# Performance work log

Measured on AMD Instinct MI355X. Metric: run time of the kernel, lower is better.

## Reference

```python
import jax, jax.numpy as jnp
import numpy as np

NUM_LAYERS = 3
DROPOUT = 0.1
N_NODES = 100000
N_EDGES = 3200000
D_FEAT = 128


def setup_inputs() -> dict:
    key = jax.random.key(0)
    k1, k2, k3, k4 = jax.random.split(key, 4)
    question_embs = jax.random.normal(k1, (N_NODES, D_FEAT), dtype=jnp.float32)
    edge_rows = jax.random.randint(k2, (N_EDGES,), 0, N_NODES, dtype=jnp.int32)
    edge_cols = jax.random.randint(k3, (N_EDGES,), 0, N_NODES, dtype=jnp.int32)
    edge_vals = jax.random.uniform(k4, (N_EDGES,), dtype=jnp.float32)
    return {"question_embs": question_embs, "edge_rows": edge_rows,
            "edge_cols": edge_cols, "edge_vals": edge_vals}


def _spmm(edge_rows, edge_cols, edge_vals, x):
    # sparse [N,N] @ dense [N,D] in COO form: out[r] += v * x[c]
    msgs = edge_vals[:, None] * x[edge_cols]        # [E, D]
    return jax.ops.segment_sum(msgs, edge_rows, num_segments=N_NODES)


def reference(question_embs, edge_rows, edge_cols, edge_vals):
    keep = 1.0 - DROPOUT
    base_key = jax.random.key(42)
    acc = question_embs                  # running sum over layer outputs
    prev = question_embs
    for layer in range(NUM_LAYERS):
        h = _spmm(edge_rows, edge_cols, edge_vals, prev)
        h = h + prev                     # residual to previous layer output
        mask = jax.random.bernoulli(jax.random.fold_in(base_key, layer),
                                    keep, h.shape)
        h = jnp.where(mask, h / keep, 0.0)  # F.dropout semantics (training)
        acc = acc + h
        prev = h
    return acc / (NUM_LAYERS + 1)        # mean over stacked layer outputs
```

## Files before the change

kernel.cpp:

```cpp
#include <hip/hip_runtime.h>
#include <stdint.h>

#define NN 100000
#define DF 128
#define NE 3200000
#define NELEM (NN * DF)
#define NBUCK 391
#define BCAP 12288
#define BSTRIDE 16
#define EPB 4096
#define NBINBLK ((NE + EPB - 1) / EPB)
#define OVF_CAP 65536

__host__ __device__ __forceinline__ void tf2x32(uint32_t& x0, uint32_t& x1,
                                                uint32_t k0, uint32_t k1) {
  uint32_t ks2 = k0 ^ k1 ^ 0x1BD11BDAu;
  x0 += k0; x1 += k1;
#define TF_RND(r) { x0 += x1; x1 = (x1 << (r)) | (x1 >> (32 - (r))); x1 ^= x0; }
  TF_RND(13) TF_RND(15) TF_RND(26) TF_RND(6)
  x0 += k1;  x1 += ks2 + 1u;
  TF_RND(17) TF_RND(29) TF_RND(16) TF_RND(24)
  x0 += ks2; x1 += k0 + 2u;
  TF_RND(13) TF_RND(15) TF_RND(26) TF_RND(6)
  x0 += k0;  x1 += k1 + 3u;
  TF_RND(17) TF_RND(29) TF_RND(16) TF_RND(24)
  x0 += k1;  x1 += ks2 + 4u;
  TF_RND(13) TF_RND(15) TF_RND(26) TF_RND(6)
  x0 += ks2; x1 += k0 + 5u;
#undef TF_RND
}

__device__ __forceinline__ bool keep_elem(uint32_t kA, uint32_t kB, uint32_t idx) {
  uint32_t x0 = 0u, x1 = idx;
  tf2x32(x0, x1, kA, kB);
  uint32_t bits = x0 ^ x1;
  float u = __uint_as_float((bits >> 9) | 0x3f800000u) - 1.0f;
  return u < 0.9f;
}

__device__ __forceinline__ uint16_t f2bf(float f) {
  uint32_t x = __float_as_uint(f);
  uint32_t r = x + 0x7fffu + ((x >> 16) & 1u);
  return (uint16_t)(r >> 16);
}

__device__ __forceinline__ uint64_t pack_edge(int row, int col, float val) {
  return ((uint64_t)(uint32_t)row << 47) | ((uint64_t)(uint32_t)col << 30) |
         (uint64_t)(__float_as_uint(val) >> 2);
}

__device__ __forceinline__ uint32_t pack_csr(int col, float v) {
  int m = (int)(v * 32768.0f + 0.5f);
  if (m > 32767) m = 32767;
  return ((uint32_t)col << 15) | (uint32_t)m;
}

__global__ __launch_bounds__(256) void binfill2_kernel(
    const int* __restrict__ rows, const int* __restrict__ cols,
    const float* __restrict__ vals,
    int* __restrict__ bcnt,
    int* __restrict__ ovf_cnt, int* __restrict__ row_cnt_ovf,
    uint64_t* __restrict__ staging, uint64_t* __restrict__ ovf) {
  __shared__ int lcnt[NBUCK];
  __shared__ int lcur[NBUCK];
  int t = threadIdx.x;
  for (int i = t; i < NBUCK; i += 256) lcnt[i] = 0;
  __syncthreads();

  int base = blockIdx.x * EPB;
  int rr[16];
#pragma unroll
  for (int k = 0; k < 16; ++k) {
    int e = base + k * 256 + t;
    rr[k] = (e < NE) ? rows[e] : -1;
    if (rr[k] >= 0) atomicAdd(&lcnt[rr[k] >> 8], 1);
  }
  __syncthreads();
  for (int i = t; i < NBUCK; i += 256)
    lcur[i] = atomicAdd(&bcnt[i * BSTRIDE], lcnt[i]);
  __syncthreads();
#pragma unroll
  for (int k = 0; k < 16; ++k) {
    if (rr[k] < 0) continue;
    int e = base + k * 256 + t;
    int row = rr[k];
    int b = row >> 8;
    uint64_t packed = pack_edge(row, cols[e], vals[e]);
    int slot = atomicAdd(&lcur[b], 1);
    if (slot < BCAP) {
      staging[(size_t)b * BCAP + slot] = packed;
    } else {
      int o = atomicAdd(ovf_cnt, 1);
      if (o < OVF_CAP) ovf[o] = packed;
      atomicAdd(&row_cnt_ovf[row], 1);
    }
  }
}

__global__ __launch_bounds__(512) void scan_bsums_kernel(const int* __restrict__ bcnt,
                                                         int* __restrict__ boff) {
  __shared__ int lds[512];
  int tid = threadIdx.x;
  int v = (tid < NBUCK) ? bcnt[tid * BSTRIDE] : 0;
  lds[tid] = v;
  __syncthreads();
#pragma unroll
  for (int off = 1; off < 512; off <<= 1) {
    int add = (tid >= off) ? lds[tid - off] : 0;
    __syncthreads();
    lds[tid] += add;
    __syncthreads();
  }
  if (tid < NBUCK) boff[tid] = lds[tid] - v;
}

__global__ __launch_bounds__(256) void scatter_csr2_kernel(
    const int* __restrict__ bcnt, const int* __restrict__ boff,
    const int* __restrict__ row_cnt_ovf,
    const uint64_t* __restrict__ staging,
    int* __restrict__ row_ptr, int* __restrict__ row_fill,
    uint32_t* __restrict__ csr) {
  __shared__ int scnt[256];
  __shared__ int lds[256];
  __shared__ int lcur[256];
  int b = blockIdx.x;
  int t = threadIdx.x;
  int g = b * 256 + t;
  int n_tot = bcnt[b * BSTRIDE];
  int n_stg = min(n_tot, BCAP);
  const uint64_t* src = staging + (size_t)b * BCAP;

  scnt[t] = 0;
  __syncthreads();
  for (int i = t; i < n_stg; i += 256)
    atomicAdd(&scnt[(int)(src[i] >> 47) & 255], 1);
  __syncthreads();
  int ovfc = (g < NN) ? row_cnt_ovf[g] : 0;
  int v = scnt[t] + ovfc;
  lds[t] = v;
  __syncthreads();
#pragma unroll
  for (int off = 1; off < 256; off <<= 1) {
    int add = (t >= off) ? lds[t - off] : 0;
    __syncthreads();
    lds[t] += add;
    __syncthreads();
  }
  int excl = lds[t] - v;
  int bo = boff[b];
  if (g <= NN) row_ptr[g] = bo + excl;
  if (g < NN) row_fill[g] = bo + excl + scnt[t];
  lcur[t] = excl;
  __syncthreads();
  for (int i = t; i < n_stg; i += 256) {
    uint64_t p = src[i];
    int rl = (int)(p >> 47) & 255;
    int col = (int)((p >> 30) & 0x1FFFFu);
    float vv = __uint_as_float(((uint32_t)p & 0x3FFFFFFFu) << 2);
    int pos = bo + atomicAdd(&lcur[rl], 1);
    csr[pos] = pack_csr(col, vv);
  }
}

__global__ __launch_bounds__(256) void ovf_drain_kernel(
    const int* __restrict__ ovf_cnt, const uint64_t* __restrict__ ovf,
    int* __restrict__ row_fill, uint32_t* __restrict__ csr) {
  int n = min(*ovf_cnt, OVF_CAP);
  for (int i = threadIdx.x; i < n; i += 256) {
    uint64_t p = ovf[i];
    int row = (int)(p >> 47);
    int col = (int)((p >> 30) & 0x1FFFFu);
    float vv = __uint_as_float(((uint32_t)p & 0x3FFFFFFFu) << 2);
    int pos = atomicAdd(&row_fill[row], 1);
    csr[pos] = pack_csr(col, vv);
  }
}

__global__ __launch_bounds__(256) void convert_kernel(const float4* __restrict__ src,
                                                      ushort4* __restrict__ dst) {
  int i = blockIdx.x * 256 + threadIdx.x;
  if (i < NELEM / 4) {
    float4 v = src[i];
    dst[i] = make_ushort4(f2bf(v.x), f2bf(v.y), f2bf(v.z), f2bf(v.w));
  }
}

template <int MODE>
__global__ __launch_bounds__(256) void spmm_layer_kernel(
    const int* __restrict__ row_ptr,
    const uint32_t* __restrict__ csr,
    const uint32_t* __restrict__ xb,
    const uint32_t* __restrict__ qb,
    const uint32_t* __restrict__ h1b,
    uint32_t* __restrict__ hb_out,
    float2* __restrict__ outv,
    uint32_t kA, uint32_t kB) {
  int r = __builtin_amdgcn_readfirstlane(blockIdx.x * 4 + (threadIdx.x >> 6));
  if (r >= NN) return;
  int lane = threadIdx.x & 63;
  int beg = row_ptr[r], end = row_ptr[r + 1];

  float s0a = 0.f, s1a = 0.f, s0b = 0.f, s1b = 0.f;
  int j = beg;
  int n8 = beg + ((end - beg) & ~7);
  for (; j < n8; j += 8) {
    uint32_t cv[8];
#pragma unroll
    for (int u = 0; u < 8; ++u) cv[u] = csr[j + u];
    uint32_t t[8];
#pragma unroll
    for (int u = 0; u < 8; ++u) {
      const uint32_t* p = xb + (size_t)(cv[u] >> 15) * 64;
      t[u] = p[lane];
    }
#pragma unroll
    for (int u = 0; u < 8; ++u) {
      float v = (float)(cv[u] & 0x7FFFu) * (1.0f / 32768.0f);
      float lo = __uint_as_float(t[u] << 16);
      float hi = __uint_as_float(t[u] & 0xFFFF0000u);
      if (u & 1) { s0b += v * lo; s1b += v * hi; }
      else       { s0a += v * lo; s1a += v * hi; }
    }
  }
  for (; j < end; ++j) {
    uint32_t cv = csr[j];
    float v = (float)(cv & 0x7FFFu) * (1.0f / 32768.0f);
    const uint32_t* p = xb + (size_t)(cv >> 15) * 64;
    uint32_t t = p[lane];
    s0a += v * __uint_as_float(t << 16);
    s1a += v * __uint_as_float(t & 0xFFFF0000u);
  }
  float s0 = s0a + s0b, s1 = s1a + s1b;

  int oi = r * 64 + lane;
  uint32_t pw = xb[oi];
  float p0 = __uint_as_float(pw << 16);
  float p1 = __uint_as_float(pw & 0xFFFF0000u);

  uint32_t base = (uint32_t)r * 128u + (uint32_t)lane * 2u;
  float t0 = s0 + p0, t1 = s1 + p1;
  float h0 = keep_elem(kA, kB, base)      ? t0 * (1.0f / 0.9f) : 0.0f;
  float h1 = keep_elem(kA, kB, base + 1u) ? t1 * (1.0f / 0.9f) : 0.0f;

  if (MODE < 2) {
    hb_out[oi] = (uint32_t)f2bf(h0) | ((uint32_t)f2bf(h1) << 16);
  } else {
    uint32_t qw = qb[oi];
    uint32_t hw = h1b[oi];
    float q0 = __uint_as_float(qw << 16), q1 = __uint_as_float(qw & 0xFFFF0000u);
    float a0 = __uint_as_float(hw << 16), a1 = __uint_as_float(hw & 0xFFFF0000u);
    outv[oi] = make_float2((q0 + a0 + p0 + h0) * 0.25f,
                           (q1 + a1 + p1 + h1) * 0.25f);
  }
}

extern "C" void kernel_launch(void* const* d_in, const int* in_sizes, int n_in,
                              void* d_out, int out_size, void* d_ws, size_t ws_size,
                              hipStream_t stream) {
  const float* q   = (const float*)d_in[0];
  const int* rows  = (const int*)d_in[1];
  const int* cols  = (const int*)d_in[2];
  const float* vls = (const float*)d_in[3];
  float* out = (float*)d_out;

  uint32_t kA[3], kB[3];
  for (int l = 0; l < 3; ++l) {
    uint32_t x0 = 0u, x1 = (uint32_t)l;
    tf2x32(x0, x1, 0u, 42u);
    kA[l] = x0; kB[l] = x1;
  }

  uint16_t* xb_q = (uint16_t*)d_ws;
  uint16_t* hb1  = xb_q + NELEM;
  uint16_t* hb2  = hb1 + NELEM;
  uint64_t* staging = (uint64_t*)hb1;
  uint32_t* csr  = (uint32_t*)(hb2 + NELEM);
  int* row_ptr   = (int*)(csr + NE);
  int* boff      = row_ptr + NN + 1;
  int* row_fill  = boff + NBUCK;
  int* row_cnt_ovf = row_fill + NN;
  int* bcnt      = row_cnt_ovf + NN;
  int* ovf_cnt   = bcnt + NBUCK * BSTRIDE;
  uint64_t* ovf  = (uint64_t*)(((uintptr_t)(ovf_cnt + 1) + 7) & ~(uintptr_t)7);

  dim3 blk(256);

  hipMemsetAsync(row_cnt_ovf, 0, (size_t)(NN + NBUCK * BSTRIDE + 1) * 4, stream);
  convert_kernel<<<NELEM / 4 / 256, blk, 0, stream>>>((const float4*)q, (ushort4*)xb_q);
  binfill2_kernel<<<NBINBLK, blk, 0, stream>>>(
      rows, cols, vls, bcnt, ovf_cnt, row_cnt_ovf, staging, ovf);
  scan_bsums_kernel<<<1, 512, 0, stream>>>(bcnt, boff);
  scatter_csr2_kernel<<<NBUCK, blk, 0, stream>>>(
      bcnt, boff, row_cnt_ovf, staging, row_ptr, row_fill, csr);
  ovf_drain_kernel<<<1, blk, 0, stream>>>(ovf_cnt, ovf, row_fill, csr);

  const int grid = NN / 4;
  spmm_layer_kernel<0><<<grid, blk, 0, stream>>>(
      row_ptr, csr, (const uint32_t*)xb_q, nullptr, nullptr,
      (uint32_t*)hb1, nullptr, kA[0], kB[0]);
  spmm_layer_kernel<1><<<grid, blk, 0, stream>>>(
      row_ptr, csr, (const uint32_t*)hb1, nullptr, nullptr,
      (uint32_t*)hb2, nullptr, kA[1], kB[1]);
  spmm_layer_kernel<2><<<grid, blk, 0, stream>>>(
      row_ptr, csr, (const uint32_t*)hb2, (const uint32_t*)xb_q,
      (const uint32_t*)hb1, nullptr, (float2*)out, kA[2], kB[2]);
}
```

Before: 445.3 us.

## Split SpMM into feature-half passes with two rows per wavefront

Each SpMM layer now runs as two launches, each covering one 64-feature half of the bf16 rows. A wavefront handles two rows at once, 32 lanes per row. The intent is to shrink the gathered working set per pass (half of each row, 128 bytes) so it stays in cache better, and to fold the value scaling out of the inner loop. The cost is reading the CSR indices twice per layer, divergent row lengths within a wavefront (the loop runs to the longer row), and twice as many launches.

```diff
diff --git a/kernel.cpp b/kernel.cpp
--- a/kernel.cpp
+++ b/kernel.cpp
@@ -185,8 +185,8 @@
   }
 }
 
-template <int MODE>
-__global__ __launch_bounds__(256) void spmm_layer_kernel(
+template <int MODE, int PASS>
+__global__ __launch_bounds__(256) void spmm_half_kernel(
     const int* __restrict__ row_ptr,
     const uint32_t* __restrict__ csr,
     const uint32_t* __restrict__ xb,
@@ -195,49 +195,65 @@
     uint32_t* __restrict__ hb_out,
     float2* __restrict__ outv,
     uint32_t kA, uint32_t kB) {
-  int r = __builtin_amdgcn_readfirstlane(blockIdx.x * 4 + (threadIdx.x >> 6));
-  if (r >= NN) return;
+  int pr = __builtin_amdgcn_readfirstlane(blockIdx.x * 4 + (threadIdx.x >> 6));
+  int rA = pr * 2;
   int lane = threadIdx.x & 63;
-  int beg = row_ptr[r], end = row_ptr[r + 1];
-
-  float s0a = 0.f, s1a = 0.f, s0b = 0.f, s1b = 0.f;
-  int j = beg;
-  int n8 = beg + ((end - beg) & ~7);
-  for (; j < n8; j += 8) {
-    uint32_t cv[8];
-#pragma unroll
-    for (int u = 0; u < 8; ++u) cv[u] = csr[j + u];
-    uint32_t t[8];
+  int l = lane & 31;
+  int half = lane >> 5;
+
+  int begA = row_ptr[rA];
+  int endA = row_ptr[rA + 1];
+  int endB = row_ptr[rA + 2];
+  int lenA = endA - begA, lenB = endB - endA;
+  const uint32_t* csrA = csr + begA;
+  const uint32_t* csrB = csr + endA;
+  int ml = lenA > lenB ? lenA : lenB;
+
+  const char* xbase = (const char*)xb;
+  uint32_t loff = (uint32_t)(PASS * 128 + (l << 2));
+
+  float s0 = 0.f, s1 = 0.f;
+  int j = 0, ml8 = ml & ~7;
+  for (; j < ml8; j += 8) {
+    uint32_t cw[8];
 #pragma unroll
     for (int u = 0; u < 8; ++u) {
-      const uint32_t* p = xb + (size_t)(cv[u] >> 15) * 64;
-      t[u] = p[lane];
+      uint32_t a = csrA[j + u]; a = (j + u < lenA) ? a : 0u;
+      uint32_t b = csrB[j + u]; b = (j + u < lenB) ? b : 0u;
+      cw[u] = half ? b : a;
     }
+    uint32_t ta[8];
 #pragma unroll
     for (int u = 0; u < 8; ++u) {
-      float v = (float)(cv[u] & 0x7FFFu) * (1.0f / 32768.0f);
-      float lo = __uint_as_float(t[u] << 16);
-      float hi = __uint_as_float(t[u] & 0xFFFF0000u);
-      if (u & 1) { s0b += v * lo; s1b += v * hi; }
-      else       { s0a += v * lo; s1a += v * hi; }
+      uint32_t off = ((cw[u] >> 15) << 8) + loff;
+      ta[u] = *(const uint32_t*)(xbase + off);
     }
-  }
-  for (; j < end; ++j) {
-    uint32_t cv = csr[j];
-    float v = (float)(cv & 0x7FFFu) * (1.0f / 32768.0f);
-    const uint32_t* p = xb + (size_t)(cv >> 15) * 64;
-    uint32_t t = p[lane];
-    s0a += v * __uint_as_float(t << 16);
-    s1a += v * __uint_as_float(t & 0xFFFF0000u);
-  }
-  float s0 = s0a + s0b, s1 = s1a + s1b;
-
-  int oi = r * 64 + lane;
+#pragma unroll
+    for (int u = 0; u < 8; ++u) {
+      float v = (float)(cw[u] & 0x7FFFu);
+      s0 += v * __uint_as_float(ta[u] << 16);
+      s1 += v * __uint_as_float(ta[u] & 0xFFFF0000u);
+    }
+  }
+  for (; j < ml; ++j) {
+    uint32_t a = csrA[j]; a = (j < lenA) ? a : 0u;
+    uint32_t b = csrB[j]; b = (j < lenB) ? b : 0u;
+    uint32_t cw = half ? b : a;
+    uint32_t t = *(const uint32_t*)(xbase + (((cw >> 15) << 8) + loff));
+    float v = (float)(cw & 0x7FFFu);
+    s0 += v * __uint_as_float(t << 16);
+    s1 += v * __uint_as_float(t & 0xFFFF0000u);
+  }
+  s0 *= (1.0f / 32768.0f);
+  s1 *= (1.0f / 32768.0f);
+
+  int r = rA + half;
+  int oi = r * 64 + PASS * 32 + l;
   uint32_t pw = xb[oi];
   float p0 = __uint_as_float(pw << 16);
   float p1 = __uint_as_float(pw & 0xFFFF0000u);
 
-  uint32_t base = (uint32_t)r * 128u + (uint32_t)lane * 2u;
+  uint32_t base = (uint32_t)r * 128u + (uint32_t)(PASS * 64) + (uint32_t)(l << 1);
   float t0 = s0 + p0, t1 = s1 + p1;
   float h0 = keep_elem(kA, kB, base)      ? t0 * (1.0f / 0.9f) : 0.0f;
   float h1 = keep_elem(kA, kB, base + 1u) ? t1 * (1.0f / 0.9f) : 0.0f;
@@ -294,14 +310,21 @@
       bcnt, boff, row_cnt_ovf, staging, row_ptr, row_fill, csr);
   ovf_drain_kernel<<<1, blk, 0, stream>>>(ovf_cnt, ovf, row_fill, csr);
 
-  const int grid = NN / 4;
-  spmm_layer_kernel<0><<<grid, blk, 0, stream>>>(
-      row_ptr, csr, (const uint32_t*)xb_q, nullptr, nullptr,
-      (uint32_t*)hb1, nullptr, kA[0], kB[0]);
-  spmm_layer_kernel<1><<<grid, blk, 0, stream>>>(
-      row_ptr, csr, (const uint32_t*)hb1, nullptr, nullptr,
-      (uint32_t*)hb2, nullptr, kA[1], kB[1]);
-  spmm_layer_kernel<2><<<grid, blk, 0, stream>>>(
-      row_ptr, csr, (const uint32_t*)hb2, (const uint32_t*)xb_q,
-      (const uint32_t*)hb1, nullptr, (float2*)out, kA[2], kB[2]);
-}
+  const int grid = NN / 2 / 4;
+  const uint32_t* xq = (const uint32_t*)xb_q;
+  uint32_t* h1 = (uint32_t*)hb1;
+  uint32_t* h2 = (uint32_t*)hb2;
+
+  spmm_half_kernel<0, 0><<<grid, blk, 0, stream>>>(
+      row_ptr, csr, xq, nullptr, nullptr, h1, nullptr, kA[0], kB[0]);
+  spmm_half_kernel<0, 1><<<grid, blk, 0, stream>>>(
+      row_ptr, csr, xq, nullptr, nullptr, h1, nullptr, kA[0], kB[0]);
+  spmm_half_kernel<1, 0><<<grid, blk, 0, stream>>>(
+      row_ptr, csr, h1, nullptr, nullptr, h2, nullptr, kA[1], kB[1]);
+  spmm_half_kernel<1, 1><<<grid, blk, 0, stream>>>(
+      row_ptr, csr, h1, nullptr, nullptr, h2, nullptr, kA[1], kB[1]);
+  spmm_half_kernel<2, 0><<<grid, blk, 0, stream>>>(
+      row_ptr, csr, h2, xq, h1, nullptr, (float2*)out, kA[2], kB[2]);
+  spmm_half_kernel<2, 1><<<grid, blk, 0, stream>>>(
+      row_ptr, csr, h2, xq, h1, nullptr, (float2*)out, kA[2], kB[2]);
+}
```

Measured after the change: 465.3 us. 4.5% more time.
